# Kernel tuning notes

Measured on AMD Instinct MI355X. Metric: run time of the kernel, lower is better.

## Reference

```python
import jax, jax.numpy as jnp
import numpy as np

E = 100   # embed_size
H = 64    # q_hidden_num
B, T, K = 64, 20, 50
I, U = 50000, 10000


def setup_inputs() -> dict:
    key = jax.random.key(0)
    ks = jax.random.split(key, 16)
    # sample_vectors: table = sigma[i]*randn + mu[i]; sigma=[1,1,1,.1,.1,1,1], mu=0
    alpha = jax.random.normal(ks[0], (I, E), jnp.float32)
    rho = jax.random.normal(ks[1], (I, E), jnp.float32)
    lam = jax.random.normal(ks[2], (I, E), jnp.float32)
    beta = 0.1 * jax.random.normal(ks[3], (I, E), jnp.float32)
    mu_tab = 0.1 * jax.random.normal(ks[4], (I, E), jnp.float32)
    theta = jax.random.normal(ks[5], (U, E), jnp.float32)
    gamma = jax.random.normal(ks[6], (U, E), jnp.float32)
    w1 = jax.random.normal(ks[7], (H, E), jnp.float32) / np.sqrt(E)
    b1 = jnp.zeros((H,), jnp.float32)
    w2 = jax.random.normal(ks[8], (1, H), jnp.float32) / np.sqrt(H)
    b2 = jnp.zeros((1,), jnp.float32)
    sigma_list = jnp.array([1.0, 1.0, 1.0, 0.1, 0.1, 1.0, 1.0], jnp.float32)
    mu_list = jnp.zeros((7,), jnp.float32)
    prices = jax.random.uniform(ks[9], (B, T), jnp.float32, 1.0, 20.0)
    price_table = jax.random.uniform(ks[10], (I,), jnp.float32, 1.0, 20.0)
    item_ids = jax.random.randint(ks[11], (B, T), 0, I, jnp.int32)
    # distinct itemset ids per row (contiguous random window)
    starts = jax.random.randint(ks[12], (B,), 0, I - K, jnp.int32)
    itemset = starts[:, None] + jnp.arange(K, dtype=jnp.int32)[None, :]
    userid = jax.random.randint(ks[13], (B,), 0, U, jnp.int32)
    return dict(alpha=alpha, rho=rho, lam=lam, beta=beta, mu_tab=mu_tab,
                theta=theta, gamma=gamma, w1=w1, b1=b1, w2=w2, b2=b2,
                sigma_list=sigma_list, mu_list=mu_list, prices=prices,
                price_table=price_table, item_ids=item_ids, itemset=itemset,
                userid=userid, batch_size=B)


def reference(alpha, rho, lam, beta, mu_tab, theta, gamma, w1, b1, w2, b2,
              sigma_list, mu_list, prices, price_table, item_ids, itemset,
              userid, batch_size):
    f32 = alpha.dtype

    def Qf(x):  # Q_function in eval mode (dropout identity)
        h = jax.nn.relu(x @ w1.T + b1)
        return jax.nn.sigmoid(h @ w2.T + b2)  # [..., 1]; mean over last dim == itself

    def prior_sum(v, idx):  # sum_e 0.5*(v-mu)*(-(v-mu)/sigma)
        return (-0.5 / sigma_list[idx]) * jnp.sum((v - mu_list[idx]) ** 2)

    th = theta[userid]   # [B,E]
    ga = gamma[userid]   # [B,E]
    a_c = alpha[itemset]; r_c = rho[itemset]; l_c = lam[itemset]
    b_c = beta[itemset]; m_c = mu_tab[itemset]          # [B,K,E]
    a0 = alpha[item_ids]; r0 = rho[item_ids]
    l0 = lam[item_ids]; b0 = beta[item_ids]             # [B,T,E]

    # ---- f prior ----
    q_l = (Qf(a_c).sum() + Qf(r_c).sum() + Qf(l_c).sum() + Qf(b_c).sum()
           + Qf(m_c).sum() + Qf(th).sum() + Qf(ga).sum())
    p_l = (prior_sum(a_c, 0) + prior_sum(r_c, 1) + prior_sum(l_c, 2)
           + prior_sum(b_c, 3) + prior_sum(m_c, 4)
           + prior_sum(th, 5) + prior_sum(ga, 6))

    # ---- kesai(item, user, price) ----
    def kes(a_i, b_i, l_i, th_b, ga_b, price):
        return (l_i.mean(-1) + (th_b * a_i).mean(-1)
                - (ga_b * b_i).mean(-1) * jnp.log(price))

    kes0 = kes(a0, b0, l0, th[:, None, :], ga[:, None, :], prices)            # [B,T]
    kesc = kes(a_c, b_c, l_c, th[:, None, :], ga[:, None, :], price_table[itemset])  # [B,K]

    # list-aliasing bug: basket at step k = [item0, c_0..c_k] (c_j skipped iff ==item0)
    m = itemset[:, None, :] != item_ids[:, :, None]     # [B,T,K]
    mf = m.astype(f32)
    S = a0[:, :, None, :] + jnp.cumsum(mf[..., None] * a_c[:, None, :, :], axis=2)  # [B,T,K,E]
    lenk = 1.0 + jnp.cumsum(mf, axis=2)                 # [B,T,K]

    D = jnp.einsum('btke,bje->btkj', S, r_c)            # rho_cj . S_k
    rda0 = jnp.einsum('bje,bte->btj', r_c, a0)          # rho_cj . alpha_item0
    A_kj = jnp.einsum('bke,bje->bkj', a_c, r_c)         # rho_cj . alpha_ck

    denom = (lenk + 1.0)[..., None] * E                 # [B,T,K,1]
    j_gt_k = jnp.arange(K)[:, None] < jnp.arange(K)[None, :]
    elig = m[:, :, None, :] & j_gt_k[None, None, :, :]  # [B,T,K,K]
    NEG = jnp.asarray(-1e30, f32)

    val0 = (D + rda0[:, :, None, :]) / denom + kesc[:, None, None, :]
    look0 = jnp.maximum(0.0, jnp.max(jnp.where(elig, val0, NEG), axis=-1))
    valc = (D + A_kj[:, None, :, :]) / denom + kesc[:, None, None, :]
    lookc = jnp.maximum(0.0, jnp.max(jnp.where(elig, valc, NEG), axis=-1))

    interact0 = jnp.einsum('bte,btke->btk', r0, S) / (E * lenk)
    interactc = jnp.einsum('bke,btke->btk', r_c, S) / (E * lenk)

    Kes0 = kes0[:, :, None] + interact0 + look0
    KesC = kesc[:, None, :] + interactc + lookc
    basket = jnp.sum(jnp.where(m, jax.nn.log_sigmoid(Kes0 - KesC), 0.0))

    # torch: loss = sum over batch; torch.mean(scalar) == scalar
    return p_l - q_l + basket
```

## Files before the change

kernel.cpp:

```cpp
#include <hip/hip_runtime.h>
#include <math.h>

#define Ee 100
#define Hh 64
#define Bb 64
#define Tt 20
#define Kk 50
#define NROWS 16128
#define NQUADS 4032
#define PREBLKS 256
#define QBLKS   512
#define NB3 (Bb*Tt)

__device__ __forceinline__ float wave_sum(float v) {
    #pragma unroll
    for (int m = 32; m >= 1; m >>= 1) v += __shfl_xor(v, m, 64);
    return v;
}
__device__ __forceinline__ float rl(float v, int l) {
    return __uint_as_float(__builtin_amdgcn_readlane(__float_as_uint(v), l));
}

__global__ __launch_bounds__(256) void k_fused1(
    const float* __restrict__ alpha, const float* __restrict__ rho,
    const float* __restrict__ lam,   const float* __restrict__ beta,
    const float* __restrict__ mu_tab,const float* __restrict__ theta,
    const float* __restrict__ gamma_,const float* __restrict__ w1,
    const float* __restrict__ b1,    const float* __restrict__ w2,
    const float* __restrict__ b2,    const float* __restrict__ sigma_list,
    const float* __restrict__ prices,const float* __restrict__ price_table,
    const int* __restrict__ item_ids,const int* __restrict__ itemset,
    const int* __restrict__ userid,
    float* __restrict__ A, float* __restrict__ rda0, float* __restrict__ ra0c,
    float* __restrict__ kesc, float* __restrict__ kes0, float* __restrict__ rda0self,
    float* __restrict__ partialQ)
{
    __shared__ float buf[12260];
    const int tid  = threadIdx.x;
    const int lane = tid & 63;
    const int wid  = tid >> 6;

    if (blockIdx.x < PREBLKS) {
        float* acT = buf;
        float* rcT = buf + 5200;
        float* a0T = buf + 10400;
        float* r0T = buf + 11200;
        float* th  = buf + 12000;
        float* ga  = buf + 12100;
        int*   iis = (int*)&buf[12200];
        int*   iid5= (int*)&buf[12252];

        const int b = blockIdx.x >> 2, q = blockIdx.x & 3;
        const int kcnt = (q < 2) ? 13 : 12;
        const int kbeg = q*12 + ((q < 2) ? q : 2);
        const int tbeg = q*5;
        const long uid = userid[b];

        if (tid < Kk) iis[tid] = itemset[b*Kk + tid];
        else if (tid >= 56 && tid < 61) iid5[tid-56] = item_ids[b*Tt + tbeg + (tid-56)];
        for (int i = tid; i < Ee; i += 256) {
            th[i] = theta[uid*Ee+i];
            ga[i] = gamma_[uid*Ee+i];
        }
        __syncthreads();

        for (int i = tid; i < 2500; i += 256) {
            int half = (i < 1250) ? 0 : 1;
            int ii = i - half*1250;
            int k = ii % Kk, c = ii / Kk;
            long idx = iis[k];
            float4 v = *(const float4*)((half ? rho : alpha) + idx*Ee + 4*c);
            float* dst = half ? rcT : acT;
            dst[(4*c+0)*52+k] = v.x; dst[(4*c+1)*52+k] = v.y;
            dst[(4*c+2)*52+k] = v.z; dst[(4*c+3)*52+k] = v.w;
        }
        for (int i = tid; i < 250; i += 256) {
            int half = (i < 125) ? 0 : 1;
            int ii = i - half*125;
            int tl = ii % 5, c = ii / 5;
            long idx = iid5[tl];
            float4 v = *(const float4*)((half ? rho : alpha) + idx*Ee + 4*c);
            float* dst = half ? r0T : a0T;
            dst[(4*c+0)*8+tl] = v.x; dst[(4*c+1)*8+tl] = v.y;
            dst[(4*c+2)*8+tl] = v.z; dst[(4*c+3)*8+tl] = v.w;
        }
        __syncthreads();

        if (tid < kcnt*13) {
            int k = kbeg + tid/13, jt = tid - (tid/13)*13, j0 = 4*jt;
            float s0=0.f, s1=0.f, s2=0.f, s3=0.f;
            #pragma unroll 4
            for (int e = 0; e < Ee; ++e) {
                float a  = acT[e*52 + k];
                float4 r = *(const float4*)&rcT[e*52 + j0];
                s0 = fmaf(a, r.x, s0); s1 = fmaf(a, r.y, s1);
                s2 = fmaf(a, r.z, s2); s3 = fmaf(a, r.w, s3);
            }
            float* dst = A + ((long)b*Kk + k)*Kk + j0;
            dst[0] = s0; dst[1] = s1;
            if (jt < 12) { dst[2] = s2; dst[3] = s3; }
        } else if (tid < kcnt*13 + 65) {
            int t2 = tid - kcnt*13;
            int tl = t2/13, jt = t2 - 13*tl, j0 = 4*jt;
            float p0=0.f,p1=0.f,p2=0.f,p3=0.f, q0=0.f,q1=0.f,q2=0.f,q3=0.f;
            #pragma unroll 4
            for (int e = 0; e < Ee; ++e) {
                float a0v = a0T[e*8 + tl];
                float r0v = r0T[e*8 + tl];
                float4 r = *(const float4*)&rcT[e*52 + j0];
                float4 a = *(const float4*)&acT[e*52 + j0];
                p0 = fmaf(r.x, a0v, p0); p1 = fmaf(r.y, a0v, p1);
                p2 = fmaf(r.z, a0v, p2); p3 = fmaf(r.w, a0v, p3);
                q0 = fmaf(r0v, a.x, q0); q1 = fmaf(r0v, a.y, q1);
                q2 = fmaf(r0v, a.z, q2); q3 = fmaf(r0v, a.w, q3);
            }
            int t = tbeg + tl;
            float* d1 = rda0 + ((long)b*Tt + t)*Kk + j0;
            float* d2 = ra0c + ((long)b*Tt + t)*Kk + j0;
            d1[0]=p0; d1[1]=p1; d2[0]=q0; d2[1]=q1;
            if (jt < 12) { d1[2]=p2; d1[3]=p3; d2[2]=q2; d2[3]=q3; }
        }

        for (int task = wid; task < 5 + kcnt; task += 4) {
            if (task < 5) {
                int tl = task, t = tbeg + tl;
                long idx = iid5[tl];
                float s=0.f, ml=0.f, mtha=0.f, mgb=0.f;
                if (lane < Kk) {
                    #pragma unroll
                    for (int u = 0; u < 2; ++u) {
                        int e = lane + u*Kk;
                        float a0v = a0T[e*8+tl], r0v = r0T[e*8+tl];
                        s    = fmaf(r0v, a0v, s);
                        ml  += lam[idx*Ee+e];
                        mtha = fmaf(th[e], a0v, mtha);
                        mgb  = fmaf(ga[e], beta[idx*Ee+e], mgb);
                    }
                }
                s = wave_sum(s); ml = wave_sum(ml); mtha = wave_sum(mtha); mgb = wave_sum(mgb);
                if (lane == 0) {
                    rda0self[b*Tt+t] = s;
                    kes0[b*Tt+t] = 0.01f*ml + 0.01f*mtha - 0.01f*mgb*logf(prices[b*Tt+t]);
                }
            } else {
                int k = kbeg + (task - 5);
                long idx = iis[k];
                float ml=0.f, mtha=0.f, mgb=0.f;
                if (lane < Kk) {
                    #pragma unroll
                    for (int u = 0; u < 2; ++u) {
                        int e = lane + u*Kk;
                        ml  += lam[idx*Ee+e];
                        mtha = fmaf(th[e], acT[e*52+k], mtha);
                        mgb  = fmaf(ga[e], beta[idx*Ee+e], mgb);
                    }
                }
                ml = wave_sum(ml); mtha = wave_sum(mtha); mgb = wave_sum(mgb);
                if (lane == 0)
                    kesc[b*Kk+k] = 0.01f*ml + 0.01f*mtha - 0.01f*mgb*logf(price_table[idx]);
            }
        }
    } else {
        float* w1s = buf;
        float* red = buf + 6400;

        for (int i = tid; i < Hh*Ee/4; i += 256)
            *(float4*)&w1s[4*i] = *(const float4*)&w1[4*i];
        __syncthreads();

        const float w2j = w2[lane];
        const float b1j = b1[lane];
        const float b2v = b2[0];
        const float c0 = -0.5f/sigma_list[0], c1 = -0.5f/sigma_list[1];
        const float c2 = -0.5f/sigma_list[2], c3 = -0.5f/sigma_list[3];
        const float c4 = -0.5f/sigma_list[4], c5 = -0.5f/sigma_list[5];
        const float c6 = -0.5f/sigma_list[6];

        const bool ldA = (lane < 25);
        const bool ldB = (lane >= 32) && (lane < 57);
        const int  lq  = ldA ? (lane<<2) : ((lane-32)<<2);
        const int  wave = (blockIdx.x - PREBLKS)*4 + wid;

        #define LOAD_QUAD(Q, AB, CD, CF)                                          \
        {                                                                         \
            int r4_ = 4*(Q);                                                      \
            const float* tab_; int4 ii_;                                          \
            if (r4_ < 16000) {                                                    \
                int seg_ = r4_/3200;                                              \
                ii_ = *(const int4*)&itemset[r4_ - seg_*3200];                    \
                tab_ = (seg_==0)?alpha:(seg_==1)?rho:(seg_==2)?lam                \
                      :(seg_==3)?beta:mu_tab;                                     \
                CF = (seg_==0)?c0:(seg_==1)?c1:(seg_==2)?c2:(seg_==3)?c3:c4;      \
            } else if (r4_ < 16064) {                                             \
                ii_ = *(const int4*)&userid[r4_-16000]; tab_ = theta;  CF = c5;   \
            } else {                                                              \
                ii_ = *(const int4*)&userid[r4_-16064]; tab_ = gamma_; CF = c6;   \
            }                                                                     \
            if (ldA) {                                                            \
                AB = *(const float4*)(tab_ + (long)ii_.x*Ee + lq);                \
                CD = *(const float4*)(tab_ + (long)ii_.z*Ee + lq);                \
            } else if (ldB) {                                                     \
                AB = *(const float4*)(tab_ + (long)ii_.y*Ee + lq);                \
                CD = *(const float4*)(tab_ + (long)ii_.w*Ee + lq);                \
            }                                                                     \
        }

        float ssacc = 0.f, qacc = 0.f;
        float4 curAB = make_float4(0.f,0.f,0.f,0.f);
        float4 curCD = make_float4(0.f,0.f,0.f,0.f);
        float  ccur = 0.f;
        int qd = wave;
        if (qd < NQUADS) LOAD_QUAD(qd, curAB, curCD, ccur);

        while (qd < NQUADS) {
            float4 nAB = make_float4(0.f,0.f,0.f,0.f);
            float4 nCD = make_float4(0.f,0.f,0.f,0.f);
            float  cnx = 0.f;
            int qn = qd + QBLKS*4;
            if (qn < NQUADS) LOAD_QUAD(qn, nAB, nCD, cnx);

            if (ldA || ldB)
                ssacc += ccur * (curAB.x*curAB.x + curAB.y*curAB.y
                               + curAB.z*curAB.z + curAB.w*curAB.w
                               + curCD.x*curCD.x + curCD.y*curCD.y
                               + curCD.z*curCD.z + curCD.w*curCD.w);

            float hA0=b1j, hA1=0.f, hB0=b1j, hB1=0.f;
            float hC0=b1j, hC1=0.f, hD0=b1j, hD1=0.f;
            #pragma unroll
            for (int i = 0; i < 25; ++i) {
                float4 wv = *(const float4*)&w1s[lane*Ee + 4*i];
                hA0 = fmaf(rl(curAB.x, i),    wv.x, hA0);
                hA1 = fmaf(rl(curAB.y, i),    wv.y, hA1);
                hA0 = fmaf(rl(curAB.z, i),    wv.z, hA0);
                hA1 = fmaf(rl(curAB.w, i),    wv.w, hA1);
                hB0 = fmaf(rl(curAB.x, 32+i), wv.x, hB0);
                hB1 = fmaf(rl(curAB.y, 32+i), wv.y, hB1);
                hB0 = fmaf(rl(curAB.z, 32+i), wv.z, hB0);
                hB1 = fmaf(rl(curAB.w, 32+i), wv.w, hB1);
                hC0 = fmaf(rl(curCD.x, i),    wv.x, hC0);
                hC1 = fmaf(rl(curCD.y, i),    wv.y, hC1);
                hC0 = fmaf(rl(curCD.z, i),    wv.z, hC0);
                hC1 = fmaf(rl(curCD.w, i),    wv.w, hC1);
                hD0 = fmaf(rl(curCD.x, 32+i), wv.x, hD0);
                hD1 = fmaf(rl(curCD.y, 32+i), wv.y, hD1);
                hD0 = fmaf(rl(curCD.z, 32+i), wv.z, hD0);
                hD1 = fmaf(rl(curCD.w, 32+i), wv.w, hD1);
            }
            float vA = fmaxf(hA0+hA1, 0.f)*w2j;
            float vB = fmaxf(hB0+hB1, 0.f)*w2j;
            float vC = fmaxf(hC0+hC1, 0.f)*w2j;
            float vD = fmaxf(hD0+hD1, 0.f)*w2j;
            #pragma unroll
            for (int m = 32; m >= 1; m >>= 1) {
                vA += __shfl_xor(vA, m, 64);
                vB += __shfl_xor(vB, m, 64);
                vC += __shfl_xor(vC, m, 64);
                vD += __shfl_xor(vD, m, 64);
            }
            qacc -= 1.f/(1.f+expf(-(vA+b2v))) + 1.f/(1.f+expf(-(vB+b2v)))
                  + 1.f/(1.f+expf(-(vC+b2v))) + 1.f/(1.f+expf(-(vD+b2v)));

            curAB = nAB; curCD = nCD; ccur = cnx; qd = qn;
        }
        #undef LOAD_QUAD

        float s = wave_sum(ssacc);
        if (lane == 0) red[wid] = s + qacc;
        __syncthreads();
        if (tid == 0)
            partialQ[blockIdx.x - PREBLKS] = red[0]+red[1]+red[2]+red[3];
    }
}

__global__ __launch_bounds__(64) void k_main(
    const float* __restrict__ A, const float* __restrict__ rda0,
    const float* __restrict__ ra0c, const float* __restrict__ kesc,
    const float* __restrict__ kes0, const float* __restrict__ rda0self,
    const int* __restrict__ item_ids, const int* __restrict__ itemset,
    float* __restrict__ partial)
{
    __shared__ float Als[Kk*51];
    __shared__ float Cum[Kk*51];
    __shared__ float2 js[Kk];

    const int bt = blockIdx.x;
    const int b  = bt / Tt;
    const int lane = threadIdx.x;

    for (int i = lane; i < Kk*Kk; i += 64) {
        int k = i / Kk;
        Als[k*51 + (i - k*Kk)] = A[(long)b*Kk*Kk + i];
    }

    const int  myitem = item_ids[bt];
    const bool valid  = lane < Kk;
    const int  cj     = valid ? itemset[b*Kk+lane] : -1;
    const bool mj     = valid && (cj != myitem);
    const unsigned long long mask = __ballot(mj);

    const float rj_own = valid ? rda0[(long)bt*Kk+lane] : 0.f;
    const float kc_own = valid ? kesc[b*Kk+lane] : 0.f;
    const float raj    = valid ? ra0c[(long)bt*Kk+lane] : 0.f;
    if (valid) js[lane] = make_float2(rj_own, kc_own);

    const unsigned mlo = (unsigned)mask, mhi = (unsigned)(mask >> 32);
    const int below = __builtin_amdgcn_mbcnt_hi(mhi, __builtin_amdgcn_mbcnt_lo(mlo, 0));
    const float len    = 1.f + (float)below + (mj ? 1.f : 0.f);
    const float invden = 1.f / ((len + 1.f) * (float)Ee);
    const float invlen = 1.f / ((float)Ee * len);

    float pv = mj ? raj : 0.f;
    #pragma unroll
    for (int off = 1; off <= 32; off <<= 1) {
        float u = __shfl_up(pv, off, 64);
        if (lane >= off) pv += u;
    }
    const float cumra  = pv;
    const float r0self = rda0self[bt];
    const float k0     = kes0[bt];

    asm volatile("s_waitcnt lgkmcnt(0)" ::: "memory");

    if (valid) {
        float cum = 0.f;
        #pragma unroll 5
        for (int k = 0; k < Kk; ++k) {
            float mfk = ((mask >> k) & 1ull) ? 1.0f : 0.0f;
            cum = fmaf(mfk, Als[k*51 + lane], cum);
            Cum[k*51 + lane] = cum;
        }
    }
    asm volatile("s_waitcnt lgkmcnt(0)" ::: "memory");

    const int lc = valid ? lane : (Kk-1);
    float max0 = -3e38f, maxc = -3e38f, diag = 0.f;
    #pragma unroll 2
    for (int j = 0; j < Kk; ++j) {
        float c = Cum[lc*51 + j];
        if (j == lane) diag = c;
        if ((mask >> j) & 1ull) {
            float  a  = Als[lc*51 + j];
            float2 sj = js[j];
            float v0 = fmaf(c + 2.f*sj.x, invden, sj.y);
            float vc = fmaf(a - sj.x,    invden, v0);
            if (lane < j) { max0 = fmaxf(max0, v0); maxc = fmaxf(maxc, vc); }
        }
    }

    float look0 = fmaxf(0.f, max0);
    float lookc = fmaxf(0.f, maxc);
    float Kes0 = k0     + fmaf(r0self + cumra, invlen, look0);
    float KesC = kc_own + fmaf(rj_own + diag,  invlen, lookc);
    float x = Kes0 - KesC;
    float term = (x >= 0.f) ? -log1pf(expf(-x)) : (x - log1pf(expf(x)));
    float contrib = mj ? term : 0.f;
    float s = wave_sum(contrib);
    if (lane == 0) partial[bt] = s;
}

__global__ __launch_bounds__(256) void k_final(
    const float* __restrict__ p1, int n1,
    const float* __restrict__ p3, int n3,
    float* __restrict__ out)
{
    __shared__ double sh[256];
    double s = 0.0;
    for (int i = threadIdx.x; i < n1; i += 256) s += (double)p1[i];
    for (int i = threadIdx.x; i < n3; i += 256) s += (double)p3[i];
    sh[threadIdx.x] = s;
    __syncthreads();
    for (int m = 128; m >= 1; m >>= 1) {
        if (threadIdx.x < m) sh[threadIdx.x] += sh[threadIdx.x + m];
        __syncthreads();
    }
    if (threadIdx.x == 0) out[0] = (float)sh[0];
}

extern "C" void kernel_launch(void* const* d_in, const int* in_sizes, int n_in,
                              void* d_out, int out_size, void* d_ws, size_t ws_size,
                              hipStream_t stream) {
    const float* alpha      = (const float*)d_in[0];
    const float* rho        = (const float*)d_in[1];
    const float* lam        = (const float*)d_in[2];
    const float* beta       = (const float*)d_in[3];
    const float* mu_tab     = (const float*)d_in[4];
    const float* theta      = (const float*)d_in[5];
    const float* gamma_     = (const float*)d_in[6];
    const float* w1         = (const float*)d_in[7];
    const float* b1         = (const float*)d_in[8];
    const float* w2         = (const float*)d_in[9];
    const float* b2         = (const float*)d_in[10];
    const float* sigma_list = (const float*)d_in[11];
    const float* prices      = (const float*)d_in[13];
    const float* price_table = (const float*)d_in[14];
    const int*   item_ids    = (const int*)d_in[15];
    const int*   itemset     = (const int*)d_in[16];
    const int*   userid      = (const int*)d_in[17];

    float* ws = (float*)d_ws;
    const size_t offA    = 0;
    const size_t offRDA  = offA   + (size_t)Bb*Kk*Kk;
    const size_t offRA0C = offRDA + (size_t)Bb*Tt*Kk;
    const size_t offKESC = offRA0C+ (size_t)Bb*Tt*Kk;
    const size_t offKES0 = offKESC+ (size_t)Bb*Kk;
    const size_t offSELF = offKES0+ (size_t)Bb*Tt;
    const size_t offP1   = offSELF+ (size_t)Bb*Tt;
    const size_t offP3   = offP1  + QBLKS;

    k_fused1<<<PREBLKS + QBLKS, 256, 0, stream>>>(
        alpha, rho, lam, beta, mu_tab, theta, gamma_,
        w1, b1, w2, b2, sigma_list, prices, price_table,
        item_ids, itemset, userid,
        ws + offA, ws + offRDA, ws + offRA0C,
        ws + offKESC, ws + offKES0, ws + offSELF,
        ws + offP1);
    k_main<<<NB3, 64, 0, stream>>>(ws + offA, ws + offRDA, ws + offRA0C,
                                   ws + offKESC, ws + offKES0, ws + offSELF,
                                   item_ids, itemset, ws + offP3);
    k_final<<<1, 256, 0, stream>>>(ws + offP1, QBLKS, ws + offP3, NB3, (float*)d_out);
}
```

Before: 36.36 us.

## Share A tile across four timesteps per block and derive masked cumsum from unmasked prefix

k_main now runs 256-thread blocks that each handle four timesteps of the same batch row, so the 50x50 A tile is loaded once per block with float4 reads and shared by four waves. Because itemset entries are distinct, at most one position matches the item; the masked cumulative sum is rebuilt from a single unmasked prefix sum minus that one row, with lengths computed in closed form. The j-loop is fully unrolled with float4 LDS reads and branchless max updates. This cuts the per-(b,t) serial cumsum and redundant global loads, but it relies on itemset rows having no duplicate ids.

```diff
diff --git a/kernel.cpp b/kernel.cpp
--- a/kernel.cpp
+++ b/kernel.cpp
@@ -273,88 +273,112 @@
     }
 }
 
-__global__ __launch_bounds__(64) void k_main(
+__global__ __launch_bounds__(256) void k_main(
     const float* __restrict__ A, const float* __restrict__ rda0,
     const float* __restrict__ ra0c, const float* __restrict__ kesc,
     const float* __restrict__ kes0, const float* __restrict__ rda0self,
     const int* __restrict__ item_ids, const int* __restrict__ itemset,
     float* __restrict__ partial)
 {
-    __shared__ float Als[Kk*51];
-    __shared__ float Cum[Kk*51];
-    __shared__ float2 js[Kk];
-
-    const int bt = blockIdx.x;
-    const int b  = bt / Tt;
-    const int lane = threadIdx.x;
-
-    for (int i = lane; i < Kk*Kk; i += 64) {
-        int k = i / Kk;
-        Als[k*51 + (i - k*Kk)] = A[(long)b*Kk*Kk + i];
-    }
-
-    const int  myitem = item_ids[bt];
-    const bool valid  = lane < Kk;
-    const int  cj     = valid ? itemset[b*Kk+lane] : -1;
-    const bool mj     = valid && (cj != myitem);
-    const unsigned long long mask = __ballot(mj);
-
-    const float rj_own = valid ? rda0[(long)bt*Kk+lane] : 0.f;
-    const float kc_own = valid ? kesc[b*Kk+lane] : 0.f;
-    const float raj    = valid ? ra0c[(long)bt*Kk+lane] : 0.f;
-    if (valid) js[lane] = make_float2(rj_own, kc_own);
-
-    const unsigned mlo = (unsigned)mask, mhi = (unsigned)(mask >> 32);
-    const int below = __builtin_amdgcn_mbcnt_hi(mhi, __builtin_amdgcn_mbcnt_lo(mlo, 0));
-    const float len    = 1.f + (float)below + (mj ? 1.f : 0.f);
-    const float invden = 1.f / ((len + 1.f) * (float)Ee);
-    const float invlen = 1.f / ((float)Ee * len);
-
-    float pv = mj ? raj : 0.f;
+    __shared__ float Als[Kk*52];
+    __shared__ float Pls[Kk*52];
+    __shared__ float rdat[4][52];
+    __shared__ float kescs[52];
+    __shared__ int   iisS[Kk];
+    __shared__ int   iidS[4];
+
+    const int bk = blockIdx.x;
+    const int b  = bk / 5;
+    const int tbase = (bk % 5) * 4;
+    const int tid = threadIdx.x;
+    const int lane = tid & 63, wid = tid >> 6;
+    const int t  = tbase + wid;
+    const int bt = b*Tt + t;
+
+    for (int i = tid; i < 625; i += 256) {
+        float4 v = *(const float4*)&A[(long)b*2500 + 4*i];
+        int m = 4*i;
+        Als[(m/50)*52 + m%50]         = v.x;
+        Als[((m+1)/50)*52 + (m+1)%50] = v.y;
+        Als[((m+2)/50)*52 + (m+2)%50] = v.z;
+        Als[((m+3)/50)*52 + (m+3)%50] = v.w;
+    }
+    if (tid < Kk) iisS[tid] = itemset[b*Kk + tid];
+    else if (tid < Kk + 4) iidS[tid - Kk] = item_ids[b*Tt + tbase + (tid - Kk)];
+
+    const bool valid = lane < Kk;
+    const float rj_own = valid ? rda0[(long)bt*Kk + lane] : 0.f;
+    const float kc_own = valid ? kesc[b*Kk + lane] : 0.f;
+    const float raj    = valid ? ra0c[(long)bt*Kk + lane] : 0.f;
+    if (valid) { rdat[wid][lane] = rj_own; kescs[lane] = kc_own; }
+    __syncthreads();
+
+    if (wid == 0 && lane < Kk) {
+        float s = 0.f;
+        #pragma unroll 5
+        for (int k = 0; k < Kk; ++k) {
+            s += Als[k*52 + lane];
+            Pls[k*52 + lane] = s;
+        }
+    }
+    __syncthreads();
+
+    const int item = iidS[wid];
+    bool eq = valid && (iisS[lane] == item);
+    unsigned long long mq = __ballot(eq);
+    int p_t = mq ? (int)__ffsll((long long)mq) - 1 : -1;
+    const int pr = (p_t < 0) ? 0 : p_t;
+
+    float pv = raj;
     #pragma unroll
     for (int off = 1; off <= 32; off <<= 1) {
         float u = __shfl_up(pv, off, 64);
         if (lane >= off) pv += u;
     }
-    const float cumra  = pv;
-    const float r0self = rda0self[bt];
-    const float k0     = kes0[bt];
-
-    asm volatile("s_waitcnt lgkmcnt(0)" ::: "memory");
-
-    if (valid) {
-        float cum = 0.f;
-        #pragma unroll 5
-        for (int k = 0; k < Kk; ++k) {
-            float mfk = ((mask >> k) & 1ull) ? 1.0f : 0.0f;
-            cum = fmaf(mfk, Als[k*51 + lane], cum);
-            Cum[k*51 + lane] = cum;
-        }
-    }
-    asm volatile("s_waitcnt lgkmcnt(0)" ::: "memory");
+    float rasub = (p_t >= 0) ? rl(raj, p_t) : 0.f;
+    const float cumra = pv - ((p_t >= 0 && lane >= p_t) ? rasub : 0.f);
+
+    const int   sub_le = (p_t >= 0 && p_t <= lane) ? 1 : 0;
+    const float len    = (float)(lane + 2 - sub_le);
+    const float invden = 1.f / ((len + 1.f) * 100.f);
+    const float invlen = 1.f / (100.f * len);
+    const float subf   = (p_t >= 0 && lane >= p_t) ? 1.f : 0.f;
 
     const int lc = valid ? lane : (Kk-1);
     float max0 = -3e38f, maxc = -3e38f, diag = 0.f;
-    #pragma unroll 2
-    for (int j = 0; j < Kk; ++j) {
-        float c = Cum[lc*51 + j];
-        if (j == lane) diag = c;
-        if ((mask >> j) & 1ull) {
-            float  a  = Als[lc*51 + j];
-            float2 sj = js[j];
-            float v0 = fmaf(c + 2.f*sj.x, invden, sj.y);
-            float vc = fmaf(a - sj.x,    invden, v0);
-            if (lane < j) { max0 = fmaxf(max0, v0); maxc = fmaxf(maxc, vc); }
-        }
-    }
-
-    float look0 = fmaxf(0.f, max0);
-    float lookc = fmaxf(0.f, maxc);
-    float Kes0 = k0     + fmaf(r0self + cumra, invlen, look0);
-    float KesC = kc_own + fmaf(rj_own + diag,  invlen, lookc);
-    float x = Kes0 - KesC;
-    float term = (x >= 0.f) ? -log1pf(expf(-x)) : (x - log1pf(expf(x)));
-    float contrib = mj ? term : 0.f;
+
+    #define PROC(JJ, P_, A_, T_, R_, K_)                               \
+    {   const int j = (JJ);                                            \
+        float Cum = fmaf(-subf, T_, P_);                               \
+        float v0 = fmaf(fmaf(2.f, R_, Cum), invden, K_);               \
+        float vc = fmaf(Cum + R_ + A_, invden, K_);                    \
+        bool elig = (j > lane) && (j != p_t) && (j < Kk);              \
+        max0 = elig ? fmaxf(max0, v0) : max0;                          \
+        maxc = elig ? fmaxf(maxc, vc) : maxc;                          \
+        if (j == lc) diag = Cum; }
+
+    #pragma unroll
+    for (int jq = 0; jq < 13; ++jq) {
+        const int j0 = 4*jq;
+        float4 Pq = *(const float4*)&Pls[lc*52 + j0];
+        float4 Aq = *(const float4*)&Als[lc*52 + j0];
+        float4 Tq = *(const float4*)&Als[pr*52 + j0];
+        float4 Rq = *(const float4*)&rdat[wid][j0];
+        float4 Kq = *(const float4*)&kescs[j0];
+        PROC(j0+0, Pq.x, Aq.x, Tq.x, Rq.x, Kq.x)
+        PROC(j0+1, Pq.y, Aq.y, Tq.y, Rq.y, Kq.y)
+        PROC(j0+2, Pq.z, Aq.z, Tq.z, Rq.z, Kq.z)
+        PROC(j0+3, Pq.w, Aq.w, Tq.w, Rq.w, Kq.w)
+    }
+    #undef PROC
+
+    const float look0 = fmaxf(0.f, max0);
+    const float lookc = fmaxf(0.f, maxc);
+    const float Kes0 = kes0[bt] + fmaf(rda0self[bt] + cumra, invlen, look0);
+    const float KesC = kc_own   + fmaf(rj_own + diag,        invlen, lookc);
+    const float x = Kes0 - KesC;
+    const float term = (x >= 0.f) ? -log1pf(expf(-x)) : (x - log1pf(expf(x)));
+    const float contrib = (valid && lane != p_t) ? term : 0.f;
     float s = wave_sum(contrib);
     if (lane == 0) partial[bt] = s;
 }
@@ -415,8 +439,8 @@
         ws + offA, ws + offRDA, ws + offRA0C,
         ws + offKESC, ws + offKES0, ws + offSELF,
         ws + offP1);
-    k_main<<<NB3, 64, 0, stream>>>(ws + offA, ws + offRDA, ws + offRA0C,
-                                   ws + offKESC, ws + offKES0, ws + offSELF,
-                                   item_ids, itemset, ws + offP3);
+    k_main<<<Bb*5, 256, 0, stream>>>(ws + offA, ws + offRDA, ws + offRA0C,
+                                     ws + offKESC, ws + offKES0, ws + offSELF,
+                                     item_ids, itemset, ws + offP3);
     k_final<<<1, 256, 0, stream>>>(ws + offP1, QBLKS, ws + offP3, NB3, (float*)d_out);
 }
```

After: 31.94 us. 1.14x faster.
